# Performance work log

Measured on AMD Instinct MI355X. Metric: run time of the kernel, lower is better.

The kernel has to match this reference:

```python
import jax, jax.numpy as jnp
import numpy as np

B, N, M, K = 2, 50000, 50000, 16
C_IN, C_ADD, C_MID = 64, 3, 16


def setup_inputs() -> dict:
    key = jax.random.key(0)
    k1, k2, k3, k4 = jax.random.split(key, 4)
    return {
        "input_features": jax.random.normal(k1, (B, N, C_IN), dtype=jnp.float32),
        "neighbor_inds": jax.random.randint(k2, (B, M, K), 0, N, dtype=jnp.int64),
        "weightnet": jax.random.normal(k3, (B, M, K, C_MID), dtype=jnp.float32),
        "additional_features": jax.random.normal(k4, (B, M, K, C_ADD), dtype=jnp.float32),
    }


def reference(input_features, neighbor_inds, weightnet, additional_features):
    # Gather neighbor features: [B, M, K, C_in]
    gathered = jax.vmap(lambda feat, idx: feat[idx])(input_features, neighbor_inds)
    # Concatenate additional per-neighbor features: [B, M, K, C_in + C_add]
    cat = jnp.concatenate([gathered, additional_features], axis=-1)
    # Weighted reduce over neighbors: [B, M, C_total, C_mid]
    out = jnp.einsum("bmkc,bmkw->bmcw", cat, weightnet)
    b, m = out.shape[:2]
    return out.reshape(b, m, -1)
```

## Files before the change

kernel.cpp:

```cpp
#include <hip/hip_runtime.h>
#include <cstdint>
#include <cstddef>


namespace {
constexpr int B_   = 2;
constexpr int N_   = 50000;
constexpr int M_   = 50000;
constexpr int K_   = 16;
constexpr int CIN  = 64;
constexpr int CADD = 3;
constexpr int CMID = 16;
constexpr int CTOT = CIN + CADD;
constexpr int COUT = CTOT * CMID;
constexpr int CPAD = 72;
constexpr int WPB  = 4;
constexpr int PAIRS = B_ * M_;
}

__global__ __launch_bounds__(256, 4)
void pconv_kernel(const float* __restrict__ feat,
                  const int*   __restrict__ inds,
                  const float* __restrict__ wnet,
                  const float* __restrict__ addf,
                  float* __restrict__ out)
{
    __shared__ alignas(16) float s_cat[WPB][K_][CPAD];
    __shared__ alignas(16) float s_wn [WPB][K_][CMID];

    const int lane = threadIdx.x & 63;
    const int wid  = threadIdx.x >> 6;
    const int gwave0 = (int)((blockIdx.x * blockDim.x + threadIdx.x) >> 6);
    const int nwaves = (int)((gridDim.x * blockDim.x) >> 6);

    float (*catw)[CPAD] = s_cat[wid];
    float (*wnw)[CMID]  = s_wn[wid];

    const int k_st = lane >> 2;
    const int q_st = lane & 3;
    const int cq   = lane >> 2;
    const int wg   = lane & 3;

    for (int p = gwave0; p < PAIRS; p += nwaves) {
        const int b = p / M_;
        const float* __restrict__ wnp  = wnet + (size_t)p * (K_ * CMID);
        const float* __restrict__ adp  = addf + (size_t)p * (K_ * CADD);
        const int*   __restrict__ idxp = inds + (size_t)p * K_;

        {
            float4 v = *reinterpret_cast<const float4*>(wnp + lane * 4);
            *reinterpret_cast<float4*>(&wnw[0][0] + lane * 4) = v;
        }
        {
            const int idx = idxp[k_st];
            const float* __restrict__ row = feat + ((size_t)b * N_ + (size_t)idx) * CIN;
            #pragma unroll
            for (int j = 0; j < 4; ++j) {
                float4 v = *reinterpret_cast<const float4*>(row + j * 16 + q_st * 4);
                *reinterpret_cast<float4*>(&catw[k_st][j * 16 + q_st * 4]) = v;
            }
        }
        if (lane < K_ * CADD) {
            const int k = lane / CADD;
            const int c = lane - k * CADD;
            catw[k][CIN + c] = adp[lane];
        }

        asm volatile("s_waitcnt lgkmcnt(0)" ::: "memory");
        __builtin_amdgcn_sched_barrier(0);

        float* __restrict__ outp = out + (size_t)p * COUT;

        float acc[4][4];
        #pragma unroll
        for (int i = 0; i < 4; ++i)
            #pragma unroll
            for (int j = 0; j < 4; ++j) acc[i][j] = 0.f;

        #pragma unroll
        for (int k = 0; k < K_; ++k) {
            float4 a = *reinterpret_cast<const float4*>(&catw[k][cq * 4]);
            float4 w = *reinterpret_cast<const float4*>(&wnw[k][wg * 4]);
            const float av[4] = {a.x, a.y, a.z, a.w};
            const float wv[4] = {w.x, w.y, w.z, w.w};
            #pragma unroll
            for (int i = 0; i < 4; ++i)
                #pragma unroll
                for (int j = 0; j < 4; ++j)
                    acc[i][j] = fmaf(av[i], wv[j], acc[i][j]);
        }

        #pragma unroll
        for (int i = 0; i < 4; ++i) {
            float4 v;
            v.x = acc[i][0]; v.y = acc[i][1]; v.z = acc[i][2]; v.w = acc[i][3];
            *reinterpret_cast<float4*>(outp + (size_t)(cq * 4 + i) * CMID + wg * 4) = v;
        }

        if (lane < CADD * CMID) {
            const int ci = lane >> 4;
            const int w  = lane & 15;
            float s = 0.f;
            #pragma unroll
            for (int k = 0; k < K_; ++k)
                s = fmaf(catw[k][CIN + ci], wnw[k][w], s);
            outp[(size_t)(CIN + ci) * CMID + w] = s;
        }
    }
}

extern "C" void kernel_launch(void* const* d_in, const int* in_sizes, int n_in,
                              void* d_out, int out_size, void* d_ws, size_t ws_size,
                              hipStream_t stream) {
    const float* feat = (const float*)d_in[0];
    const int*   inds = (const int*)d_in[1];
    const float* wnet = (const float*)d_in[2];
    const float* addf = (const float*)d_in[3];
    float* outp = (float*)d_out;

    dim3 grid(2048);
    dim3 block(256);
    hipLaunchKernelGGL(pconv_kernel, grid, block, 0, stream,
                       feat, inds, wnet, addf, outp);
}
```

Baseline: 180.7 us.

## Compute per-point weighted reduction with bf16 MFMA instead of FP32 FMAs

Replaces the scalar FP32 outer-product accumulation with a 16x16x32 bf16 MFMA per 16-channel tile, staging transposed bf16 features in LDS. Gathers now use one scalar load per neighbor per lane, and the weightnet is fed straight from registers. The aim is to cut ALU and LDS work per point. The trade-offs are bf16 rounding of inputs, which lowers accuracy, and scattered scalar output stores that replace float4 stores.

```diff
diff --git a/kernel.cpp b/kernel.cpp
--- a/kernel.cpp
+++ b/kernel.cpp
@@ -4,122 +4,130 @@
 
 
 namespace {
-constexpr int B_   = 2;
-constexpr int N_   = 50000;
-constexpr int M_   = 50000;
-constexpr int K_   = 16;
-constexpr int CIN  = 64;
-constexpr int CADD = 3;
-constexpr int CMID = 16;
-constexpr int CTOT = CIN + CADD;
-constexpr int COUT = CTOT * CMID;
-constexpr int CPAD = 72;
-constexpr int WPB  = 4;
+constexpr int B_    = 2;
+constexpr int N_    = 50000;
+constexpr int M_    = 50000;
+constexpr int KNB   = 16;
+constexpr int CIN   = 64;
+constexpr int CADD  = 3;
+constexpr int CMID  = 16;
+constexpr int COUT  = 67 * CMID;
 constexpr int PAIRS = B_ * M_;
+constexpr int ROWS  = 80;
+constexpr int RS    = 40;
+constexpr int WPB   = 4;
+}
+
+typedef short short8 __attribute__((ext_vector_type(8)));
+typedef float f32x4  __attribute__((ext_vector_type(4)));
+
+static __device__ __forceinline__ unsigned short f2bf(float x) {
+  unsigned u = __builtin_bit_cast(unsigned, x);
+  u = (u + 0x7FFFu + ((u >> 16) & 1u)) >> 16;
+  return (unsigned short)u;
 }
 
 __global__ __launch_bounds__(256, 4)
-void pconv_kernel(const float* __restrict__ feat,
-                  const int*   __restrict__ inds,
-                  const float* __restrict__ wnet,
-                  const float* __restrict__ addf,
-                  float* __restrict__ out)
+void pconv_mfma(const float* __restrict__ feat,
+                const int*   __restrict__ inds,
+                const float* __restrict__ wnet,
+                const float* __restrict__ addf,
+                float* __restrict__ out)
 {
-    __shared__ alignas(16) float s_cat[WPB][K_][CPAD];
-    __shared__ alignas(16) float s_wn [WPB][K_][CMID];
+  __shared__ unsigned short s_cat[WPB][ROWS * RS];
 
-    const int lane = threadIdx.x & 63;
-    const int wid  = threadIdx.x >> 6;
-    const int gwave0 = (int)((blockIdx.x * blockDim.x + threadIdx.x) >> 6);
-    const int nwaves = (int)((gridDim.x * blockDim.x) >> 6);
+  const int lane = threadIdx.x & 63;
+  const int wid  = threadIdx.x >> 6;
+  unsigned short* catw = s_cat[wid];
 
-    float (*catw)[CPAD] = s_cat[wid];
-    float (*wnw)[CMID]  = s_wn[wid];
+  for (int i = lane; i < ROWS * RS; i += 64) catw[i] = 0;
 
-    const int k_st = lane >> 2;
-    const int q_st = lane & 3;
-    const int cq   = lane >> 2;
-    const int wg   = lane & 3;
+  const int gw = (int)((blockIdx.x * blockDim.x + threadIdx.x) >> 6);
+  const int nw = (int)((gridDim.x * blockDim.x) >> 6);
 
-    for (int p = gwave0; p < PAIRS; p += nwaves) {
-        const int b = p / M_;
-        const float* __restrict__ wnp  = wnet + (size_t)p * (K_ * CMID);
-        const float* __restrict__ adp  = addf + (size_t)p * (K_ * CADD);
-        const int*   __restrict__ idxp = inds + (size_t)p * K_;
+  const int rr = lane & 15;
+  const int g  = lane >> 4;
 
-        {
-            float4 v = *reinterpret_cast<const float4*>(wnp + lane * 4);
-            *reinterpret_cast<float4*>(&wnw[0][0] + lane * 4) = v;
-        }
-        {
-            const int idx = idxp[k_st];
-            const float* __restrict__ row = feat + ((size_t)b * N_ + (size_t)idx) * CIN;
-            #pragma unroll
-            for (int j = 0; j < 4; ++j) {
-                float4 v = *reinterpret_cast<const float4*>(row + j * 16 + q_st * 4);
-                *reinterpret_cast<float4*>(&catw[k_st][j * 16 + q_st * 4]) = v;
-            }
-        }
-        if (lane < K_ * CADD) {
-            const int k = lane / CADD;
-            const int c = lane - k * CADD;
-            catw[k][CIN + c] = adp[lane];
-        }
+  for (int p0 = gw; p0 < PAIRS; p0 += nw) {
+    const int p = __builtin_amdgcn_readfirstlane(p0);
+    const int b = p / M_;
+    const int*   __restrict__ idxp = inds + (size_t)p * KNB;
+    const float* __restrict__ wnp  = wnet + (size_t)p * (KNB * CMID);
+    const float* __restrict__ adp  = addf + (size_t)p * (KNB * CADD);
+    float*       __restrict__ outp = out  + (size_t)p * COUT;
+    const float* __restrict__ fb   = feat + (size_t)b * N_ * CIN;
 
-        asm volatile("s_waitcnt lgkmcnt(0)" ::: "memory");
-        __builtin_amdgcn_sched_barrier(0);
+    float fv[KNB];
+    #pragma unroll
+    for (int k = 0; k < KNB; ++k) {
+      const int idx = idxp[k];
+      fv[k] = fb[(size_t)idx * CIN + lane];
+    }
 
-        float* __restrict__ outp = out + (size_t)p * COUT;
+    float bw[8];
+    if (lane < 32) {
+      #pragma unroll
+      for (int j = 0; j < 8; ++j)
+        bw[j] = wnp[(g * 8 + j) * CMID + rr];
+    } else {
+      #pragma unroll
+      for (int j = 0; j < 8; ++j) bw[j] = 0.f;
+    }
 
-        float acc[4][4];
+    float av = 0.f;
+    if (lane < KNB * CADD) av = adp[lane];
+
+    short8 lo, hi;
+    #pragma unroll
+    for (int j = 0; j < 8; ++j) {
+      lo[j] = (short)f2bf(fv[j]);
+      hi[j] = (short)f2bf(fv[8 + j]);
+    }
+    *reinterpret_cast<short8*>(&catw[lane * RS])     = lo;
+    *reinterpret_cast<short8*>(&catw[lane * RS + 8]) = hi;
+
+    if (lane < KNB * CADD) {
+      const int k  = lane / 3;
+      const int c2 = lane - k * 3;
+      catw[(CIN + c2) * RS + k] = f2bf(av);
+    }
+
+    short8 bfrag;
+    #pragma unroll
+    for (int j = 0; j < 8; ++j) bfrag[j] = (short)f2bf(bw[j]);
+
+    asm volatile("s_waitcnt lgkmcnt(0)" ::: "memory");
+
+    #pragma unroll
+    for (int t = 0; t < 5; ++t) {
+      const short8 a =
+          *reinterpret_cast<const short8*>(&catw[(t * 16 + rr) * RS + g * 8]);
+      f32x4 acc = {0.f, 0.f, 0.f, 0.f};
+      acc = __builtin_amdgcn_mfma_f32_16x16x32_bf16(a, bfrag, acc, 0, 0, 0);
+      if (t < 4) {
         #pragma unroll
-        for (int i = 0; i < 4; ++i)
-            #pragma unroll
-            for (int j = 0; j < 4; ++j) acc[i][j] = 0.f;
-
+        for (int r = 0; r < 4; ++r)
+          outp[(t * 16 + g * 4 + r) * CMID + rr] = acc[r];
+      } else if (g == 0) {
         #pragma unroll
-        for (int k = 0; k < K_; ++k) {
-            float4 a = *reinterpret_cast<const float4*>(&catw[k][cq * 4]);
-            float4 w = *reinterpret_cast<const float4*>(&wnw[k][wg * 4]);
-            const float av[4] = {a.x, a.y, a.z, a.w};
-            const float wv[4] = {w.x, w.y, w.z, w.w};
-            #pragma unroll
-            for (int i = 0; i < 4; ++i)
-                #pragma unroll
-                for (int j = 0; j < 4; ++j)
-                    acc[i][j] = fmaf(av[i], wv[j], acc[i][j]);
-        }
-
-        #pragma unroll
-        for (int i = 0; i < 4; ++i) {
-            float4 v;
-            v.x = acc[i][0]; v.y = acc[i][1]; v.z = acc[i][2]; v.w = acc[i][3];
-            *reinterpret_cast<float4*>(outp + (size_t)(cq * 4 + i) * CMID + wg * 4) = v;
-        }
-
-        if (lane < CADD * CMID) {
-            const int ci = lane >> 4;
-            const int w  = lane & 15;
-            float s = 0.f;
-            #pragma unroll
-            for (int k = 0; k < K_; ++k)
-                s = fmaf(catw[k][CIN + ci], wnw[k][w], s);
-            outp[(size_t)(CIN + ci) * CMID + w] = s;
-        }
+        for (int r = 0; r < 3; ++r)
+          outp[(CIN + r) * CMID + rr] = acc[r];
+      }
     }
+  }
 }
 
 extern "C" void kernel_launch(void* const* d_in, const int* in_sizes, int n_in,
                               void* d_out, int out_size, void* d_ws, size_t ws_size,
                               hipStream_t stream) {
-    const float* feat = (const float*)d_in[0];
-    const int*   inds = (const int*)d_in[1];
-    const float* wnet = (const float*)d_in[2];
-    const float* addf = (const float*)d_in[3];
-    float* outp = (float*)d_out;
+  const float* feat = (const float*)d_in[0];
+  const int*   inds = (const int*)d_in[1];
+  const float* wnet = (const float*)d_in[2];
+  const float* addf = (const float*)d_in[3];
+  float* outp = (float*)d_out;
 
-    dim3 grid(2048);
-    dim3 block(256);
-    hipLaunchKernelGGL(pconv_kernel, grid, block, 0, stream,
-                       feat, inds, wnet, addf, outp);
+  dim3 grid(2048);
+  dim3 block(256);
+  hipLaunchKernelGGL(pconv_mfma, grid, block, 0, stream,
+                     feat, inds, wnet, addf, outp);
 }
```

After: 182.5 us. No clear change (+1.0%).
